# Kernel tuning notes

Hardware: AMD Instinct MI355X
Metric: run time of the kernel (lower is better)

Reference implementation:

```python
import jax, jax.numpy as jnp
import numpy as np

B, C, D, N, NCLS = 2048, 96, 384, 200000, 10
LN_EPS = 1e-5


def setup_inputs() -> dict:
    key = jax.random.key(0)
    ks = jax.random.split(key, 16)
    s = 0.05  # keep squared-distance logits in a sane range
    inp = {
        'k': jax.random.normal(ks[0], (B, D), jnp.float32) * s,
        'context_idx': jax.random.randint(ks[1], (B, C), 0, N),
        'candidate_embeddings': jax.random.normal(ks[2], (N, D), jnp.float32) * s,
        'candidate_y': jax.random.randint(ks[3], (N,), 0, NCLS),
        # learned params
        'label_emb': jax.random.normal(ks[4], (NCLS, D), jnp.float32) * 0.02,
        'ln_g': jnp.ones((D,), jnp.float32),
        'ln_b': jnp.zeros((D,), jnp.float32),
        'kp_w1': jax.random.normal(ks[5], (D, D), jnp.float32) * (1.0 / np.sqrt(D)),
        'kp_b1': jnp.zeros((D,), jnp.float32),
        'kp_w2': jax.random.normal(ks[6], (D, D), jnp.float32) * (1.0 / np.sqrt(D)),
        'kp_b2': jnp.zeros((D,), jnp.float32),
        'pw1': jax.random.normal(ks[7], (D, D), jnp.float32) * (1.0 / np.sqrt(D)),
        'pb1': jnp.zeros((D,), jnp.float32),
        'pw2': jax.random.normal(ks[8], (D, NCLS), jnp.float32) * (1.0 / np.sqrt(D)),
        'pb2': jnp.zeros((NCLS,), jnp.float32),
    }
    return inp


def reference(k, context_idx, candidate_embeddings, candidate_y,
              label_emb, ln_g, ln_b, kp_w1, kp_b1, kp_w2, kp_b2,
              pw1, pb1, pw2, pb2):
    # gather context (irregular access): [B, C, D], [B, C]
    context_k = candidate_embeddings[context_idx]
    context_y = candidate_y[context_idx]

    # negative squared distance via kernel trick: -|k|^2 + 2 k.ck - |ck|^2
    sim = (-jnp.sum(k * k, axis=-1, keepdims=True)
           + 2.0 * jnp.einsum('bd,bcd->bc', k, context_k)
           - jnp.sum(context_k * context_k, axis=-1))  # [B, C]
    probs = jax.nn.softmax(sim, axis=-1)  # dropout is identity in eval mode

    context_y_emb = label_emb[context_y]  # [B, C, D]

    # key_proj: LayerNorm -> Linear -> SiLU -> Linear, residual (d_main==n_out)
    def key_proj(x):
        mu = jnp.mean(x, axis=-1, keepdims=True)
        var = jnp.mean(jnp.square(x - mu), axis=-1, keepdims=True)
        h = (x - mu) * jax.lax.rsqrt(var + LN_EPS) * ln_g + ln_b
        h = jax.nn.silu(h @ kp_w1 + kp_b1)
        h = h @ kp_w2 + kp_b2
        return x + h

    # Abl == -1 branch: values = label_emb + key_proj(k - context_k)
    values = context_y_emb + key_proj(k[:, None, :] - context_k)  # [B, C, D]

    # probs[:, None] @ values -> weighted sum over context
    context_x = jnp.einsum('bc,bcd->bd', probs, values)
    x = k + context_x

    # predictor MLP (no residual: d_main != n_classes)
    h = jax.nn.silu(x @ pw1 + pb1)
    y = h @ pw2 + pb2
    return y
```

## Files before the change

kernel.cpp:

```cpp
#include <hip/hip_runtime.h>
#include <hip/hip_bf16.h>

#define BB   2048
#define CC   96
#define DD   384
#define NCLSS 10
#define AS_STRIDE 392

typedef __attribute__((ext_vector_type(8))) __bf16 bf16x8;
typedef __attribute__((ext_vector_type(4))) float  floatx4;
typedef unsigned int  uint32;
typedef unsigned short ushort16;

__device__ __forceinline__ float bflo(uint32 u){ return __uint_as_float(u << 16); }
__device__ __forceinline__ float bfhi(uint32 u){ return __uint_as_float(u & 0xffff0000u); }
__device__ __forceinline__ float bf1(ushort16 s){ return __uint_as_float(((uint32)s) << 16); }
__device__ __forceinline__ ushort16 f2bf(float f){
  uint32 u = __float_as_uint(f);
  return (ushort16)((u + 0x7fffu + ((u >> 16) & 1u)) >> 16);
}
__device__ __forceinline__ int probe_f32(const void* lng_raw){
  return (((const uint32*)lng_raw)[0] == 0x3F800000u) ? 1 : 0;
}
__device__ __forceinline__ float ld1(const void* p, size_t i, int isf32){
  return isf32 ? ((const float*)p)[i] : bf1(((const ushort16*)p)[i]);
}
__device__ __forceinline__ void ld6(const void* base, size_t row_elems, int lane, int isf32, float v[6]){
  if (isf32){
    const float2* p = (const float2*)((const float*)base + row_elems) + (size_t)lane*3;
    float2 a = p[0], b = p[1], c = p[2];
    v[0]=a.x; v[1]=a.y; v[2]=b.x; v[3]=b.y; v[4]=c.x; v[5]=c.y;
  } else {
    const uint32* p = (const uint32*)((const ushort16*)base + row_elems) + (size_t)lane*3;
    uint32 a = p[0], b = p[1], c = p[2];
    v[0]=bflo(a); v[1]=bfhi(a); v[2]=bflo(b); v[3]=bfhi(b); v[4]=bflo(c); v[5]=bfhi(c);
  }
}

__global__ __launch_bounds__(256) void k_canon(
    const void* w1, const void* w2, const void* pw1, const void* lng,
    ushort16* __restrict__ wW1T, ushort16* __restrict__ cw2,
    ushort16* __restrict__ cpw1)
{
  int isf32 = probe_f32(lng);
  int e = blockIdx.x * 256 + threadIdx.x;
  const int DW = DD * DD;
  if (e < DW) {
    int n = e / DD, kk = e % DD;
    wW1T[e] = f2bf(ld1(w1, (size_t)kk * DD + n, isf32));
    return;
  }
  e -= DW;
  if (e < DW) { cw2[e]  = f2bf(ld1(w2,  e, isf32)); return; }
  e -= DW;
  if (e < DW) { cpw1[e] = f2bf(ld1(pw1, e, isf32)); return; }
}

__device__ __forceinline__ void process_row(
    int c, const float cv[6], const float kv[6], const float gv[6], const float bvv[6],
    ushort16* As, float* sims, float* muv, float* sigv, int lane)
{
  float dv[6], s1 = 0.f, s2 = 0.f;
  #pragma unroll
  for (int j = 0; j < 6; j++) { dv[j] = kv[j] - cv[j]; s1 += dv[j]; s2 += dv[j]*dv[j]; }
  #pragma unroll
  for (int m = 32; m; m >>= 1) { s1 += __shfl_xor(s1, m); s2 += __shfl_xor(s2, m); }
  float mu = s1 * (1.f/DD);
  float var = s2 * (1.f/DD) - mu*mu;
  float rsig = rsqrtf(var + 1e-5f);
  if (lane == 0) { sims[c] = -s2; muv[c] = mu; sigv[c] = sqrtf(var + 1e-5f); }
  uint32 wa[3];
  #pragma unroll
  for (int p = 0; p < 3; p++) {
    float a0 = (dv[2*p]   - mu) * rsig * gv[2*p]   + bvv[2*p];
    float a1 = (dv[2*p+1] - mu) * rsig * gv[2*p+1] + bvv[2*p+1];
    wa[p] = (uint32)f2bf(a0) | ((uint32)f2bf(a1) << 16);
  }
  uint32* ap = (uint32*)As + c * (AS_STRIDE/2) + lane * 3;
  ap[0] = wa[0]; ap[1] = wa[1]; ap[2] = wa[2];
}

__global__ __launch_bounds__(512, 4) void k_fused(
    const void* kptr, const int* __restrict__ cidx,
    const void* cand, const int* __restrict__ cy,
    const void* lng, const void* lnb, const void* b1,
    const ushort16* __restrict__ w1t,
    float* __restrict__ wxpre, float* __restrict__ wpl, float* __restrict__ wsum)
{
  int isf32 = probe_f32(lng);
  int b = blockIdx.x;
  int tid = threadIdx.x, wave = tid >> 6, lane = tid & 63;
  __shared__ __align__(16) ushort16 As[CC * AS_STRIDE];
  __shared__ float sims[CC], probs[CC], muv[CC], sigv[CC], plbuf[NCLSS];

  float kv[6], gv[6], bvv[6];
  ld6(kptr, (size_t)b * DD, lane, isf32, kv);
  ld6(lng, 0, lane, isf32, gv);
  ld6(lnb, 0, lane, isf32, bvv);
  if (tid < NCLSS) plbuf[tid] = 0.f;

  #pragma unroll 1
  for (int i = 0; i < 12; i += 2) {
    int c0 = wave * 12 + i, c1 = c0 + 1;
    int idx0 = cidx[b * CC + c0], idx1 = cidx[b * CC + c1];
    float cv0[6], cv1[6];
    ld6(cand, (size_t)idx0 * DD, lane, isf32, cv0);
    ld6(cand, (size_t)idx1 * DD, lane, isf32, cv1);
    process_row(c0, cv0, kv, gv, bvv, As, sims, muv, sigv, lane);
    process_row(c1, cv1, kv, gv, bvv, As, sims, muv, sigv, lane);
  }
  __syncthreads();

  if (wave == 0) {
    float v0 = sims[lane];
    float v1 = (lane < 32) ? sims[lane + 64] : -1e30f;
    float mx = fmaxf(v0, v1);
    #pragma unroll
    for (int m = 32; m; m >>= 1) mx = fmaxf(mx, __shfl_xor(mx, m));
    float e0 = __expf(v0 - mx);
    float e1 = (lane < 32) ? __expf(v1 - mx) : 0.f;
    float s = e0 + e1;
    #pragma unroll
    for (int m = 32; m; m >>= 1) s += __shfl_xor(s, m);
    float inv = 1.f / s;
    probs[lane] = e0 * inv;
    if (lane < 32) probs[lane + 64] = e1 * inv;
  }
  __syncthreads();

  if (tid < CC) atomicAdd(&plbuf[cy[cidx[b * CC + tid]]], probs[tid]);

  if (tid < DD) {
    float T = 0.f, S1 = 0.f, Smu = 0.f;
    for (int c = 0; c < CC; c++) {
      float p = probs[c], ps = p * sigv[c];
      T  += ps * bf1(As[c * AS_STRIDE + tid]);
      S1 += ps;
      Smu += p * muv[c];
    }
    float gj = ld1(lng, tid, isf32), bj = ld1(lnb, tid, isf32);
    wxpre[(size_t)b * DD + tid] =
        ld1(kptr, (size_t)b * DD + tid, isf32) + (T - bj * S1) / gj + Smu;
  }
  __syncthreads();
  if (tid < NCLSS) wpl[b * NCLSS + tid] = plbuf[tid];

  int col = lane & 15, quad = lane >> 4;
  int n0 = wave * 48;
  floatx4 acc[6][3];
  #pragma unroll
  for (int i = 0; i < 6; i++)
    #pragma unroll
    for (int j = 0; j < 3; j++) acc[i][j] = (floatx4)0.f;

  #pragma unroll 2
  for (int kt = 0; kt < 12; kt++) {
    bf16x8 bfrag[3];
    #pragma unroll
    for (int tn = 0; tn < 3; tn++)
      bfrag[tn] = *(const bf16x8*)(w1t + (size_t)(n0 + tn*16 + col) * DD + kt*32 + quad*8);
    #pragma unroll
    for (int tm = 0; tm < 6; tm++) {
      bf16x8 afrag = *(const bf16x8*)(As + (tm*16 + col) * AS_STRIDE + kt*32 + quad*8);
      #pragma unroll
      for (int tn = 0; tn < 3; tn++)
        acc[tm][tn] = __builtin_amdgcn_mfma_f32_16x16x32_bf16(afrag, bfrag[tn], acc[tm][tn], 0, 0, 0);
    }
  }

  #pragma unroll
  for (int tn = 0; tn < 3; tn++) {
    int n = n0 + tn*16 + col;
    float bias = ld1(b1, n, isf32);
    float val = 0.f;
    #pragma unroll
    for (int tm = 0; tm < 6; tm++) {
      #pragma unroll
      for (int r = 0; r < 4; r++) {
        int row = tm*16 + quad*4 + r;
        float h = acc[tm][tn][r] + bias;
        h = h / (1.f + __expf(-h));
        val += probs[row] * h;
      }
    }
    val += __shfl_xor(val, 16);
    val += __shfl_xor(val, 32);
    if (quad == 0) wsum[(size_t)b * DD + n] = val;
  }
}

__global__ __launch_bounds__(384) void k_final(
    const float* __restrict__ wxpre, const float* __restrict__ wsum,
    const float* __restrict__ wpl, const void* lemb,
    const ushort16* __restrict__ cw2, const void* b2,
    const ushort16* __restrict__ cpw1, const void* pb1,
    const void* pw2, const void* pb2,
    const void* lng_raw, void* out)
{
  int isf32 = probe_f32(lng_raw);
  int b = blockIdx.x, t = threadIdx.x, lane = t & 63;
  __shared__ float shA[DD], shB[DD], shpl[NCLSS], yacc[NCLSS];
  shA[t] = wsum[(size_t)b * DD + t];
  if (t < NCLSS) { shpl[t] = wpl[b * NCLSS + t]; yacc[t] = 0.f; }
  __syncthreads();

  float a0 = 0.f, a1 = 0.f;
  #pragma unroll 8
  for (int kq = 0; kq < DD; kq += 2) {
    a0 += shA[kq]   * bf1(cw2[kq * DD + t]);
    a1 += shA[kq+1] * bf1(cw2[(kq+1) * DD + t]);
  }
  float acc = wxpre[(size_t)b * DD + t] + ld1(b2, t, isf32) + a0 + a1;
  #pragma unroll
  for (int j = 0; j < NCLSS; j++) acc += shpl[j] * ld1(lemb, j * DD + t, isf32);
  shB[t] = acc;
  __syncthreads();

  float c0 = 0.f, c1 = 0.f;
  #pragma unroll 8
  for (int kq = 0; kq < DD; kq += 2) {
    c0 += shB[kq]   * bf1(cpw1[kq * DD + t]);
    c1 += shB[kq+1] * bf1(cpw1[(kq+1) * DD + t]);
  }
  float acc2 = ld1(pb1, t, isf32) + c0 + c1;
  acc2 = acc2 / (1.f + __expf(-acc2));

  #pragma unroll
  for (int n = 0; n < NCLSS; n++) {
    float v = acc2 * ld1(pw2, (size_t)t * NCLSS + n, isf32);
    #pragma unroll
    for (int m = 32; m; m >>= 1) v += __shfl_xor(v, m);
    if (lane == 0) atomicAdd(&yacc[n], v);
  }
  __syncthreads();
  if (t < NCLSS) {
    float y = yacc[t] + ld1(pb2, t, isf32);
    if (isf32) ((float*)out)[b * NCLSS + t] = y;
    else       ((ushort16*)out)[b * NCLSS + t] = f2bf(y);
  }
}

extern "C" void kernel_launch(void* const* d_in, const int* in_sizes, int n_in,
                              void* d_out, int out_size, void* d_ws, size_t ws_size,
                              hipStream_t stream) {
  const void* kptr = d_in[0];
  const int*  cidx = (const int*)d_in[1];
  const void* cand = d_in[2];
  const int*  cy   = (const int*)d_in[3];
  const void* lemb = d_in[4];
  const void* lng  = d_in[5];
  const void* lnb  = d_in[6];
  const void* w1   = d_in[7];
  const void* b1   = d_in[8];
  const void* w2   = d_in[9];
  const void* b2   = d_in[10];
  const void* pw1  = d_in[11];
  const void* pb1  = d_in[12];
  const void* pw2  = d_in[13];
  const void* pb2  = d_in[14];

  char* ws = (char*)d_ws;
  ushort16* wW1T  = (ushort16*)(ws);
  ushort16* cw2   = (ushort16*)(ws + 294912);
  ushort16* cpw1  = (ushort16*)(ws + 589824);
  float*    wxpre = (float*)   (ws + 884736);
  float*    wpl   = (float*)   (ws + 4030464);
  float*    wsum  = (float*)   (ws + 4112384);

  int tot = DD*DD*3;
  k_canon<<<(tot + 255)/256, 256, 0, stream>>>(w1, w2, pw1, lng, wW1T, cw2, cpw1);
  k_fused<<<BB, 512, 0, stream>>>(kptr, cidx, cand, cy, lng, lnb, b1, wW1T,
                                  wxpre, wpl, wsum);
  k_final<<<BB, 384, 0, stream>>>(wxpre, wsum, wpl, lemb, cw2, b2,
                                  cpw1, pb1, pw2, pb2, lng, d_out);
}
```

Baseline: 617.4 us.

## Batch final MLP via MFMA, tile-transpose weights, prefetch gathers and B fragments

The final kernel now handles 8 batch rows per block and runs the two 384x384 matmuls with bf16 MFMA on transposed weights, instead of one row per block with scalar dot products. This removes the per-row full weight reads. The weight canonicalization now transposes all three matrices through a shared-memory tile. The fused kernel double-buffers the candidate-row gathers and the W1 B-fragment loads, and computes the weighted LN sum per wave with shared atomics. Wasting half of each 16-row MFMA tile and adding atomic contention are the tradeoffs.

Result: faster. 598.9 us (-3.0%).

```diff
diff --git a/kernel.cpp b/kernel.cpp
--- a/kernel.cpp
+++ b/kernel.cpp
@@ -39,36 +39,30 @@
 
 __global__ __launch_bounds__(256) void k_canon(
     const void* w1, const void* w2, const void* pw1, const void* lng,
-    ushort16* __restrict__ wW1T, ushort16* __restrict__ cw2,
-    ushort16* __restrict__ cpw1)
+    ushort16* __restrict__ wW1T, ushort16* __restrict__ wW2T,
+    ushort16* __restrict__ wPW1T)
 {
   int isf32 = probe_f32(lng);
-  int e = blockIdx.x * 256 + threadIdx.x;
-  const int DW = DD * DD;
-  if (e < DW) {
-    int n = e / DD, kk = e % DD;
-    wW1T[e] = f2bf(ld1(w1, (size_t)kk * DD + n, isf32));
-    return;
-  }
-  e -= DW;
-  if (e < DW) { cw2[e]  = f2bf(ld1(w2,  e, isf32)); return; }
-  e -= DW;
-  if (e < DW) { cpw1[e] = f2bf(ld1(pw1, e, isf32)); return; }
-}
-
-__device__ __forceinline__ void process_row(
-    int c, const float cv[6], const float kv[6], const float gv[6], const float bvv[6],
-    ushort16* As, float* sims, float* muv, float* sigv, int lane)
-{
-  float dv[6], s1 = 0.f, s2 = 0.f;
-  #pragma unroll
-  for (int j = 0; j < 6; j++) { dv[j] = kv[j] - cv[j]; s1 += dv[j]; s2 += dv[j]*dv[j]; }
-  #pragma unroll
-  for (int m = 32; m; m >>= 1) { s1 += __shfl_xor(s1, m); s2 += __shfl_xor(s2, m); }
-  float mu = s1 * (1.f/DD);
-  float var = s2 * (1.f/DD) - mu*mu;
-  float rsig = rsqrtf(var + 1e-5f);
-  if (lane == 0) { sims[c] = -s2; muv[c] = mu; sigv[c] = sqrtf(var + 1e-5f); }
+  int m  = blockIdx.x / 144;
+  int t  = blockIdx.x % 144;
+  int tr = t / 12, tc = t % 12;
+  const void* src = (m == 0) ? w1 : (m == 1) ? w2 : pw1;
+  ushort16* dst   = (m == 0) ? wW1T : (m == 1) ? wW2T : wPW1T;
+  __shared__ float tile[32][33];
+  int tx = threadIdx.x & 31, ty = threadIdx.x >> 5;
+  #pragma unroll
+  for (int p = 0; p < 4; p++)
+    tile[p*8 + ty][tx] = ld1(src, (size_t)(tr*32 + p*8 + ty) * DD + tc*32 + tx, isf32);
+  __syncthreads();
+  #pragma unroll
+  for (int p = 0; p < 4; p++)
+    dst[(size_t)(tc*32 + p*8 + ty) * DD + tr*32 + tx] = f2bf(tile[tx][p*8 + ty]);
+}
+
+__device__ __forceinline__ void store_row(
+    int c, const float dv[6], float mu, float rsig,
+    const float gv[6], const float bvv[6], ushort16* As, int lane)
+{
   uint32 wa[3];
   #pragma unroll
   for (int p = 0; p < 3; p++) {
@@ -78,6 +72,34 @@
   }
   uint32* ap = (uint32*)As + c * (AS_STRIDE/2) + lane * 3;
   ap[0] = wa[0]; ap[1] = wa[1]; ap[2] = wa[2];
+}
+
+__device__ __forceinline__ void process_pair(
+    int c0, const float a[6], const float b[6],
+    const float kv[6], const float gv[6], const float bvv[6],
+    ushort16* As, float* sims, float* muv, float* sigv, int lane)
+{
+  float da[6], db[6];
+  float s1a=0.f, s2a=0.f, s1b=0.f, s2b=0.f;
+  #pragma unroll
+  for (int j = 0; j < 6; j++) {
+    da[j] = kv[j] - a[j]; s1a += da[j]; s2a += da[j]*da[j];
+    db[j] = kv[j] - b[j]; s1b += db[j]; s2b += db[j]*db[j];
+  }
+  #pragma unroll
+  for (int m = 32; m; m >>= 1) {
+    s1a += __shfl_xor(s1a, m); s2a += __shfl_xor(s2a, m);
+    s1b += __shfl_xor(s1b, m); s2b += __shfl_xor(s2b, m);
+  }
+  float mua = s1a * (1.f/DD), vara = s2a * (1.f/DD) - mua*mua;
+  float mub = s1b * (1.f/DD), varb = s2b * (1.f/DD) - mub*mub;
+  float rsa = rsqrtf(vara + 1e-5f), rsb = rsqrtf(varb + 1e-5f);
+  if (lane == 0) {
+    sims[c0] = -s2a;   muv[c0] = mua;   sigv[c0] = sqrtf(vara + 1e-5f);
+    sims[c0+1] = -s2b; muv[c0+1] = mub; sigv[c0+1] = sqrtf(varb + 1e-5f);
+  }
+  store_row(c0,   da, mua, rsa, gv, bvv, As, lane);
+  store_row(c0+1, db, mub, rsb, gv, bvv, As, lane);
 }
 
 __global__ __launch_bounds__(512, 4) void k_fused(
@@ -91,23 +113,34 @@
   int b = blockIdx.x;
   int tid = threadIdx.x, wave = tid >> 6, lane = tid & 63;
   __shared__ __align__(16) ushort16 As[CC * AS_STRIDE];
-  __shared__ float sims[CC], probs[CC], muv[CC], sigv[CC], plbuf[NCLSS];
+  __shared__ float sims[CC], probs[CC], muv[CC], sigv[CC];
+  __shared__ float plbuf[NCLSS], xacc[DD], sacc[2];
+
+  if (tid < NCLSS) plbuf[tid] = 0.f;
+  if (tid < DD)    xacc[tid]  = 0.f;
+  if (tid < 2)     sacc[tid]  = 0.f;
 
   float kv[6], gv[6], bvv[6];
   ld6(kptr, (size_t)b * DD, lane, isf32, kv);
   ld6(lng, 0, lane, isf32, gv);
   ld6(lnb, 0, lane, isf32, bvv);
-  if (tid < NCLSS) plbuf[tid] = 0.f;
-
+
+  int idxs[12];
+  #pragma unroll
+  for (int t = 0; t < 12; t++) idxs[t] = cidx[b * CC + wave * 12 + t];
+
+  float cva[2][6], cvb[2][6];
+  ld6(cand, (size_t)idxs[0] * DD, lane, isf32, cva[0]);
+  ld6(cand, (size_t)idxs[1] * DD, lane, isf32, cvb[0]);
   #pragma unroll 1
-  for (int i = 0; i < 12; i += 2) {
-    int c0 = wave * 12 + i, c1 = c0 + 1;
-    int idx0 = cidx[b * CC + c0], idx1 = cidx[b * CC + c1];
-    float cv0[6], cv1[6];
-    ld6(cand, (size_t)idx0 * DD, lane, isf32, cv0);
-    ld6(cand, (size_t)idx1 * DD, lane, isf32, cv1);
-    process_row(c0, cv0, kv, gv, bvv, As, sims, muv, sigv, lane);
-    process_row(c1, cv1, kv, gv, bvv, As, sims, muv, sigv, lane);
+  for (int ip = 0; ip < 6; ip++) {
+    int cur = ip & 1, nxt = cur ^ 1;
+    if (ip < 5) {
+      ld6(cand, (size_t)idxs[2*ip+2] * DD, lane, isf32, cva[nxt]);
+      ld6(cand, (size_t)idxs[2*ip+3] * DD, lane, isf32, cvb[nxt]);
+    }
+    process_pair(wave*12 + 2*ip, cva[cur], cvb[cur], kv, gv, bvv,
+                 As, sims, muv, sigv, lane);
   }
   __syncthreads();
 
@@ -129,20 +162,32 @@
   __syncthreads();
 
   if (tid < CC) atomicAdd(&plbuf[cy[cidx[b * CC + tid]]], probs[tid]);
+  {
+    float T0=0,T1=0,T2=0,T3=0,T4=0,T5=0, S1p=0, Smup=0;
+    #pragma unroll
+    for (int i = 0; i < 12; i++) {
+      int c = wave * 12 + i;
+      float p = probs[c], ps = p * sigv[c];
+      const uint32* ap = (const uint32*)As + c * (AS_STRIDE/2) + lane * 3;
+      uint32 a0 = ap[0], a1 = ap[1], a2 = ap[2];
+      T0 += ps*bflo(a0); T1 += ps*bfhi(a0); T2 += ps*bflo(a1);
+      T3 += ps*bfhi(a1); T4 += ps*bflo(a2); T5 += ps*bfhi(a2);
+      S1p += ps; Smup += p * muv[c];
+    }
+    int j0 = lane * 6;
+    atomicAdd(&xacc[j0+0], T0); atomicAdd(&xacc[j0+1], T1);
+    atomicAdd(&xacc[j0+2], T2); atomicAdd(&xacc[j0+3], T3);
+    atomicAdd(&xacc[j0+4], T4); atomicAdd(&xacc[j0+5], T5);
+    if (lane == 0) { atomicAdd(&sacc[0], S1p); atomicAdd(&sacc[1], Smup); }
+  }
+  __syncthreads();
 
   if (tid < DD) {
-    float T = 0.f, S1 = 0.f, Smu = 0.f;
-    for (int c = 0; c < CC; c++) {
-      float p = probs[c], ps = p * sigv[c];
-      T  += ps * bf1(As[c * AS_STRIDE + tid]);
-      S1 += ps;
-      Smu += p * muv[c];
-    }
     float gj = ld1(lng, tid, isf32), bj = ld1(lnb, tid, isf32);
     wxpre[(size_t)b * DD + tid] =
-        ld1(kptr, (size_t)b * DD + tid, isf32) + (T - bj * S1) / gj + Smu;
-  }
-  __syncthreads();
+        ld1(kptr, (size_t)b * DD + tid, isf32)
+        + (xacc[tid] - bj * sacc[0]) / gj + sacc[1];
+  }
   if (tid < NCLSS) wpl[b * NCLSS + tid] = plbuf[tid];
 
   int col = lane & 15, quad = lane >> 4;
@@ -153,19 +198,28 @@
     #pragma unroll
     for (int j = 0; j < 3; j++) acc[i][j] = (floatx4)0.f;
 
-  #pragma unroll 2
+  const ushort16* wbase = w1t + (size_t)(n0 + col) * DD + quad * 8;
+  bf16x8 bcur[3];
+  #pragma unroll
+  for (int tn = 0; tn < 3; tn++)
+    bcur[tn] = *(const bf16x8*)(wbase + (size_t)tn * 16 * DD);
+  #pragma unroll 1
   for (int kt = 0; kt < 12; kt++) {
-    bf16x8 bfrag[3];
-    #pragma unroll
-    for (int tn = 0; tn < 3; tn++)
-      bfrag[tn] = *(const bf16x8*)(w1t + (size_t)(n0 + tn*16 + col) * DD + kt*32 + quad*8);
+    bf16x8 bnxt[3];
+    if (kt < 11) {
+      #pragma unroll
+      for (int tn = 0; tn < 3; tn++)
+        bnxt[tn] = *(const bf16x8*)(wbase + (size_t)tn * 16 * DD + (kt+1) * 32);
+    }
     #pragma unroll
     for (int tm = 0; tm < 6; tm++) {
       bf16x8 afrag = *(const bf16x8*)(As + (tm*16 + col) * AS_STRIDE + kt*32 + quad*8);
       #pragma unroll
       for (int tn = 0; tn < 3; tn++)
-        acc[tm][tn] = __builtin_amdgcn_mfma_f32_16x16x32_bf16(afrag, bfrag[tn], acc[tm][tn], 0, 0, 0);
-    }
+        acc[tm][tn] = __builtin_amdgcn_mfma_f32_16x16x32_bf16(afrag, bcur[tn], acc[tm][tn], 0, 0, 0);
+    }
+    #pragma unroll
+    for (int tn = 0; tn < 3; tn++) bcur[tn] = bnxt[tn];
   }
 
   #pragma unroll
@@ -189,54 +243,124 @@
   }
 }
 
-__global__ __launch_bounds__(384) void k_final(
+__global__ __launch_bounds__(512) void k_final(
     const float* __restrict__ wxpre, const float* __restrict__ wsum,
     const float* __restrict__ wpl, const void* lemb,
-    const ushort16* __restrict__ cw2, const void* b2,
-    const ushort16* __restrict__ cpw1, const void* pb1,
+    const ushort16* __restrict__ w2t, const void* b2,
+    const ushort16* __restrict__ pw1t, const void* pb1,
     const void* pw2, const void* pb2,
     const void* lng_raw, void* out)
 {
   int isf32 = probe_f32(lng_raw);
-  int b = blockIdx.x, t = threadIdx.x, lane = t & 63;
-  __shared__ float shA[DD], shB[DD], shpl[NCLSS], yacc[NCLSS];
-  shA[t] = wsum[(size_t)b * DD + t];
-  if (t < NCLSS) { shpl[t] = wpl[b * NCLSS + t]; yacc[t] = 0.f; }
-  __syncthreads();
-
-  float a0 = 0.f, a1 = 0.f;
-  #pragma unroll 8
-  for (int kq = 0; kq < DD; kq += 2) {
-    a0 += shA[kq]   * bf1(cw2[kq * DD + t]);
-    a1 += shA[kq+1] * bf1(cw2[(kq+1) * DD + t]);
-  }
-  float acc = wxpre[(size_t)b * DD + t] + ld1(b2, t, isf32) + a0 + a1;
-  #pragma unroll
-  for (int j = 0; j < NCLSS; j++) acc += shpl[j] * ld1(lemb, j * DD + t, isf32);
-  shB[t] = acc;
-  __syncthreads();
-
-  float c0 = 0.f, c1 = 0.f;
-  #pragma unroll 8
-  for (int kq = 0; kq < DD; kq += 2) {
-    c0 += shB[kq]   * bf1(cpw1[kq * DD + t]);
-    c1 += shB[kq+1] * bf1(cpw1[(kq+1) * DD + t]);
-  }
-  float acc2 = ld1(pb1, t, isf32) + c0 + c1;
-  acc2 = acc2 / (1.f + __expf(-acc2));
-
-  #pragma unroll
-  for (int n = 0; n < NCLSS; n++) {
-    float v = acc2 * ld1(pw2, (size_t)t * NCLSS + n, isf32);
-    #pragma unroll
-    for (int m = 32; m; m >>= 1) v += __shfl_xor(v, m);
-    if (lane == 0) atomicAdd(&yacc[n], v);
-  }
-  __syncthreads();
-  if (t < NCLSS) {
-    float y = yacc[t] + ld1(pb2, t, isf32);
-    if (isf32) ((float*)out)[b * NCLSS + t] = y;
-    else       ((ushort16*)out)[b * NCLSS + t] = f2bf(y);
+  int b0 = blockIdx.x * 8;
+  int tid = threadIdx.x, wave = tid >> 6, lane = tid & 63;
+  int cn = lane & 15, quad = lane >> 4;
+  __shared__ __align__(16) ushort16 As[16 * AS_STRIDE];
+  __shared__ float hbuf[8][AS_STRIDE];
+  __shared__ float lembsh[NCLSS * DD];
+  __shared__ float plsh[8][NCLSS];
+  __shared__ float part[480];
+
+  for (int e = tid; e < 16 * AS_STRIDE; e += 512) {
+    int r = e / AS_STRIDE, j = e - r * AS_STRIDE;
+    ushort16 v = (ushort16)0;
+    if (r < 8 && j < DD) v = f2bf(wsum[(size_t)(b0 + r) * DD + j]);
+    As[e] = v;
+  }
+  for (int e = tid; e < NCLSS * DD; e += 512) lembsh[e] = ld1(lemb, e, isf32);
+  if (tid < 80) plsh[tid / NCLSS][tid % NCLSS] = wpl[(b0 + tid / NCLSS) * NCLSS + tid % NCLSS];
+  __syncthreads();
+
+  int n0 = wave * 48;
+  floatx4 acc[3];
+  #pragma unroll
+  for (int j = 0; j < 3; j++) acc[j] = (floatx4)0.f;
+  const ushort16* wb2 = w2t + (size_t)(n0 + cn) * DD + quad * 8;
+  #pragma unroll 2
+  for (int kt = 0; kt < 12; kt++) {
+    bf16x8 afrag = *(const bf16x8*)(As + cn * AS_STRIDE + kt*32 + quad*8);
+    #pragma unroll
+    for (int tn = 0; tn < 3; tn++) {
+      bf16x8 bfrag = *(const bf16x8*)(wb2 + (size_t)tn * 16 * DD + kt * 32);
+      acc[tn] = __builtin_amdgcn_mfma_f32_16x16x32_bf16(afrag, bfrag, acc[tn], 0, 0, 0);
+    }
+  }
+  float xv[3][4];
+  #pragma unroll
+  for (int tn = 0; tn < 3; tn++) {
+    int n = n0 + tn*16 + cn;
+    float bb = ld1(b2, n, isf32);
+    #pragma unroll
+    for (int r = 0; r < 4; r++) {
+      int row = quad*4 + r;
+      if (row < 8) {
+        float v = acc[tn][r] + bb + wxpre[(size_t)(b0 + row) * DD + n];
+        #pragma unroll
+        for (int l = 0; l < NCLSS; l++) v += plsh[row][l] * lembsh[l * DD + n];
+        xv[tn][r] = v;
+      }
+    }
+  }
+  __syncthreads();
+  #pragma unroll
+  for (int tn = 0; tn < 3; tn++) {
+    int n = n0 + tn*16 + cn;
+    #pragma unroll
+    for (int r = 0; r < 4; r++) {
+      int row = quad*4 + r;
+      if (row < 8) As[row * AS_STRIDE + n] = f2bf(xv[tn][r]);
+    }
+  }
+  __syncthreads();
+
+  floatx4 acc2[3];
+  #pragma unroll
+  for (int j = 0; j < 3; j++) acc2[j] = (floatx4)0.f;
+  const ushort16* wbp = pw1t + (size_t)(n0 + cn) * DD + quad * 8;
+  #pragma unroll 2
+  for (int kt = 0; kt < 12; kt++) {
+    bf16x8 afrag = *(const bf16x8*)(As + cn * AS_STRIDE + kt*32 + quad*8);
+    #pragma unroll
+    for (int tn = 0; tn < 3; tn++) {
+      bf16x8 bfrag = *(const bf16x8*)(wbp + (size_t)tn * 16 * DD + kt * 32);
+      acc2[tn] = __builtin_amdgcn_mfma_f32_16x16x32_bf16(afrag, bfrag, acc2[tn], 0, 0, 0);
+    }
+  }
+  #pragma unroll
+  for (int tn = 0; tn < 3; tn++) {
+    int n = n0 + tn*16 + cn;
+    float bb = ld1(pb1, n, isf32);
+    #pragma unroll
+    for (int r = 0; r < 4; r++) {
+      int row = quad*4 + r;
+      if (row < 8) {
+        float h = acc2[tn][r] + bb;
+        hbuf[row][n] = h / (1.f + __expf(-h));
+      }
+    }
+  }
+  __syncthreads();
+
+  if (tid < 480) {
+    int r = tid / 60, rem = tid % 60, n = rem / 6, s = rem % 6;
+    float pp = 0.f;
+    int jb = s * 64;
+    #pragma unroll 8
+    for (int jj = 0; jj < 64; jj++) {
+      int j = jb + jj;
+      pp += hbuf[r][j] * ld1(pw2, (size_t)j * NCLSS + n, isf32);
+    }
+    part[tid] = pp;
+  }
+  __syncthreads();
+  if (tid < 80) {
+    int r = tid / NCLSS, n = tid % NCLSS;
+    float y = ld1(pb2, n, isf32);
+    #pragma unroll
+    for (int s = 0; s < 6; s++) y += part[r*60 + n*6 + s];
+    size_t o = (size_t)(b0 + r) * NCLSS + n;
+    if (isf32) ((float*)out)[o] = y;
+    else       ((ushort16*)out)[o] = f2bf(y);
   }
 }
 
@@ -261,16 +385,15 @@
 
   char* ws = (char*)d_ws;
   ushort16* wW1T  = (ushort16*)(ws);
-  ushort16* cw2   = (ushort16*)(ws + 294912);
-  ushort16* cpw1  = (ushort16*)(ws + 589824);
+  ushort16* wW2T  = (ushort16*)(ws + 294912);
+  ushort16* wPW1T = (ushort16*)(ws + 589824);
   float*    wxpre = (float*)   (ws + 884736);
   float*    wpl   = (float*)   (ws + 4030464);
   float*    wsum  = (float*)   (ws + 4112384);
 
-  int tot = DD*DD*3;
-  k_canon<<<(tot + 255)/256, 256, 0, stream>>>(w1, w2, pw1, lng, wW1T, cw2, cpw1);
+  k_canon<<<432, 256, 0, stream>>>(w1, w2, pw1, lng, wW1T, wW2T, wPW1T);
   k_fused<<<BB, 512, 0, stream>>>(kptr, cidx, cand, cy, lng, lnb, b1, wW1T,
                                   wxpre, wpl, wsum);
-  k_final<<<BB, 384, 0, stream>>>(wxpre, wsum, wpl, lemb, cw2, b2,
-                                  cpw1, pb1, pw2, pb2, lng, d_out);
-}
+  k_final<<<256, 512, 0, stream>>>(wxpre, wsum, wpl, lemb, wW2T, b2,
+                                   wPW1T, pb1, pw2, pb2, lng, d_out);
+}
```
